# Kernel optimization log

Measured on AMD Instinct MI355X. Metric: run time of the kernel, lower is better.

## Reference

```python
import jax, jax.numpy as jnp
import numpy as np

B_SZ, SEQ, H, P = 4, 8192, 512, 256


def _s5(x, lam_re, lam_im, log_dt, b_re, b_im, c_re, c_im, d):
    """Single-direction S5 diagonal SSM. x: [B,L,H] -> y: [B,L,H]."""
    lam = lam_re + 1j * lam_im                      # [P] complex diagonal A
    dt = jnp.exp(log_dt)                            # [P] ZOH timestep
    a_bar = jnp.exp(lam * dt)                       # [P] discretized A
    b_bar = ((a_bar - 1.0) / lam)[:, None] * (b_re + 1j * b_im)  # [P,H]
    bu = jnp.einsum('blh,ph->blp', x.astype(b_bar.dtype), b_bar)  # [B,L,P]
    a_el = jnp.broadcast_to(a_bar, bu.shape)        # time-invariant A per step

    def comb(e1, e2):  # associative combine for linear recurrence
        a1, s1 = e1
        a2, s2 = e2
        return (a1 * a2, a2 * s1 + s2)

    _, states = jax.lax.associative_scan(comb, (a_el, bu), axis=1)  # [B,L,P]
    c = c_re + 1j * c_im                            # [H,P]
    return jnp.einsum('blp,hp->blh', states, c).real + x * d


def setup_inputs() -> dict:
    key = jax.random.key(0)
    ks = jax.random.split(key, 10)
    return {
        'x': jax.random.normal(ks[0], (B_SZ, SEQ, H), dtype=jnp.float32),
        'Lambda_re': -0.1 - 0.5 * jax.random.uniform(ks[1], (2, P), dtype=jnp.float32),
        'Lambda_im': jnp.pi * jax.random.normal(ks[2], (2, P), dtype=jnp.float32),
        'log_dt': jnp.log(0.001) + (jnp.log(0.1) - jnp.log(0.001)) * jax.random.uniform(ks[3], (2, P), dtype=jnp.float32),
        'B_re': jax.random.normal(ks[4], (2, P, H), dtype=jnp.float32) / np.sqrt(H),
        'B_im': jax.random.normal(ks[5], (2, P, H), dtype=jnp.float32) / np.sqrt(H),
        'C_re': jax.random.normal(ks[6], (2, H, P), dtype=jnp.float32) / np.sqrt(P),
        'C_im': jax.random.normal(ks[7], (2, H, P), dtype=jnp.float32) / np.sqrt(P),
        'D': jax.random.normal(ks[8], (2, H), dtype=jnp.float32),
    }


def reference(x, Lambda_re, Lambda_im, log_dt, B_re, B_im, C_re, C_im, D):
    # fwd(x) + flip(bwd(flip(x)))
    y_f = _s5(x, Lambda_re[0], Lambda_im[0], log_dt[0], B_re[0], B_im[0], C_re[0], C_im[0], D[0])
    x_r = x[:, ::-1]
    y_b = _s5(x_r, Lambda_re[1], Lambda_im[1], log_dt[1], B_re[1], B_im[1], C_re[1], C_im[1], D[1])[:, ::-1]
    return y_f + y_b
```

## Files before the change

kernel.cpp:

```cpp
#include <hip/hip_runtime.h>
#include <math.h>

typedef unsigned short ushort_t;
typedef __bf16 bf16x8 __attribute__((ext_vector_type(8)));
typedef ushort_t ushort8v __attribute__((ext_vector_type(8)));
typedef float f32x4 __attribute__((ext_vector_type(4)));

#define B_SZ   4
#define SEQ    8192
#define M_ROWS (B_SZ * SEQ)
#define CH     32
#define NC     (SEQ / CH)

__device__ __forceinline__ ushort_t f2bf(float f) {
    unsigned u = __float_as_uint(f);
    u = u + 0x7fffu + ((u >> 16) & 1u);
    return (ushort_t)(u >> 16);
}
__device__ __forceinline__ float bf2f(ushort_t b) {
    return __uint_as_float(((unsigned)b) << 16);
}

__device__ __forceinline__ void load16_lds(const void* g, void* l) {
    __builtin_amdgcn_global_load_lds(
        (const __attribute__((address_space(1))) unsigned int*)g,
        (__attribute__((address_space(3))) unsigned int*)l, 16, 0, 0);
}

__global__ void prep_kernel(const float* __restrict__ Lre,
                            const float* __restrict__ Lim,
                            const float* __restrict__ ldt,
                            const float* __restrict__ Bre,
                            const float* __restrict__ Bim,
                            const float* __restrict__ Cre,
                            const float* __restrict__ Cim,
                            float* __restrict__ abar,
                            float* __restrict__ apow,
                            ushort_t* __restrict__ Bmat,
                            ushort_t* __restrict__ Cmat) {
    int idx = blockIdx.x * 256 + threadIdx.x;
    int h = idx & 511;
    int p = (idx >> 9) & 255;
    int d = idx >> 17;
    int ip = d * 256 + p;
    float lr = Lre[ip], li = Lim[ip];
    float dt = expf(ldt[ip]);
    float e   = expf(lr * dt);
    float ang = li * dt;
    float ar = e * cosf(ang), ai = e * sinf(ang);
    float nr = ar - 1.0f, ni = ai;
    float den = lr * lr + li * li;
    float cr = (nr * lr + ni * li) / den;
    float ci = (ni * lr - nr * li) / den;
    float br = Bre[idx], bi = Bim[idx];
    Bmat[(d * 512 + 2 * p) * 512 + h]     = f2bf(cr * br - ci * bi);
    Bmat[(d * 512 + 2 * p + 1) * 512 + h] = f2bf(cr * bi + ci * br);
    if (h == 0) {
        int o = d * 512 + 2 * p;
        abar[o] = ar;  abar[o + 1] = ai;
        float eC = expf(lr * dt * (float)CH);
        float aC = ang * (float)CH;
        apow[o] = eC * cosf(aC);  apow[o + 1] = eC * sinf(aC);
    }
    int p2 = idx & 255;
    int h2 = (idx >> 8) & 511;
    int d2 = idx >> 17;
    Cmat[h2 * 1024 + d2 * 512 + 2 * p2]     = f2bf(Cre[idx]);
    Cmat[h2 * 1024 + d2 * 512 + 2 * p2 + 1] = f2bf(-Cim[idx]);
}

__global__ void conv_x_kernel(const float* __restrict__ x,
                              ushort_t* __restrict__ X16) {
    int i = blockIdx.x * 256 + threadIdx.x;
    float4 v = ((const float4*)x)[i];
    ushort_t o[4] = {f2bf(v.x), f2bf(v.y), f2bf(v.z), f2bf(v.w)};
    *(uint2*)&X16[(size_t)i * 4] = *(const uint2*)o;
}

template<int EPI, int KD_, int NT>
__global__ __launch_bounds__(256)
void gemm_mfma(const ushort_t* __restrict__ A, const ushort_t* __restrict__ Bm,
               ushort_t* __restrict__ Cb, float* __restrict__ Cf,
               const float* __restrict__ X, const float* __restrict__ Dv) {
    __shared__ ushort_t As[128 * 32];
    __shared__ ushort_t Bs[128 * 32];
    const int tid  = threadIdx.x;
    const int lane = tid & 63;
    const int wv   = tid >> 6;
    const int wrow = wv >> 1, wcol = wv & 1;
    const int l15  = lane & 15, lq = lane >> 4;

    const int lin = blockIdx.x;
    const int xcd = lin & 7;
    const int j   = lin >> 3;
    const int mt  = xcd * 32 + j / NT;
    const int nt  = j % NT;
    const int m0 = mt * 128;
    const int n0 = nt * 128;
    const int CN = NT * 128;

    f32x4 acc[4][4];
#pragma unroll
    for (int i = 0; i < 4; ++i)
#pragma unroll
        for (int jj = 0; jj < 4; ++jj)
            acc[i][jj] = (f32x4){0.f, 0.f, 0.f, 0.f};

    const int grow_l = lane >> 2;
    const int gk8    = (lane & 3) * 8;

    const ushort_t* aF = As + (wrow * 64 + l15) * 32 + lq * 8;
    const ushort_t* bF = Bs + (wcol * 64 + l15) * 32 + lq * 8;

    for (int kt = 0; kt < KD_; kt += 32) {
        __syncthreads();
#pragma unroll
        for (int j2 = 0; j2 < 2; ++j2) {
            const int r0 = j2 * 64 + wv * 16;
            load16_lds(&A[(size_t)(m0 + r0 + grow_l) * KD_ + kt + gk8],
                       (void*)&As[r0 * 32]);
            load16_lds(&Bm[(size_t)(n0 + r0 + grow_l) * KD_ + kt + gk8],
                       (void*)&Bs[r0 * 32]);
        }
        __syncthreads();

        bf16x8 af[4], bfr[4];
#pragma unroll
        for (int mi = 0; mi < 4; ++mi) {
            union { ushort8v u; bf16x8 b; } cv;
            cv.u = *(const ushort8v*)(aF + mi * 512);
            af[mi] = cv.b;
        }
#pragma unroll
        for (int ni = 0; ni < 4; ++ni) {
            union { ushort8v u; bf16x8 b; } cv;
            cv.u = *(const ushort8v*)(bF + ni * 512);
            bfr[ni] = cv.b;
        }
#pragma unroll
        for (int mi = 0; mi < 4; ++mi)
#pragma unroll
            for (int ni = 0; ni < 4; ++ni)
                acc[mi][ni] = __builtin_amdgcn_mfma_f32_16x16x32_bf16(
                    af[mi], bfr[ni], acc[mi][ni], 0, 0, 0);
    }

#pragma unroll
    for (int mi = 0; mi < 4; ++mi) {
#pragma unroll
        for (int ni = 0; ni < 4; ++ni) {
            const int col = n0 + wcol * 64 + ni * 16 + l15;
            float dsum = 0.f;
            if (EPI == 1) dsum = Dv[col] + Dv[512 + col];
#pragma unroll
            for (int r = 0; r < 4; ++r) {
                const int row = m0 + wrow * 64 + mi * 16 + lq * 4 + r;
                if (EPI == 0) {
                    Cb[(size_t)row * CN + col] = f2bf(acc[mi][ni][r]);
                } else {
                    const size_t idx = (size_t)row * 512 + col;
                    Cf[idx] = acc[mi][ni][r] + X[idx] * dsum;
                }
            }
        }
    }
}

__global__ __launch_bounds__(512)
void scan_carry(const ushort_t* __restrict__ S, const float* __restrict__ abar,
                float* __restrict__ carry) {
    int b = blockIdx.x, c = blockIdx.y, t = threadIdx.x;
    int dir = t >> 8, p = t & 255;
    float ar = abar[dir * 512 + 2 * p], ai = abar[dir * 512 + 2 * p + 1];
    float sr = 0.f, si = 0.f;
    const ushort_t* base = S + ((size_t)b * SEQ + (size_t)c * CH) * 1024
                             + dir * 512 + 2 * p;
    for (int batch = 0; batch < CH; batch += 8) {
        unsigned v[8];
#pragma unroll
        for (int q = 0; q < 8; ++q) {
            int l = batch + q;
            int row = dir ? (CH - 1 - l) : l;
            v[q] = *(const unsigned*)(base + (size_t)row * 1024);
        }
#pragma unroll
        for (int q = 0; q < 8; ++q) {
            float re = bf2f((ushort_t)(v[q] & 0xffffu));
            float im = bf2f((ushort_t)(v[q] >> 16));
            float nr = fmaf(ar, sr, fmaf(-ai, si, re));
            float ni = fmaf(ar, si, fmaf(ai, sr, im));
            sr = nr; si = ni;
        }
    }
    int o = (b * NC + c) * 1024 + dir * 512 + 2 * p;
    carry[o] = sr; carry[o + 1] = si;
}

__global__ __launch_bounds__(512)
void scan_comb(const float* __restrict__ carry, float* __restrict__ init,
               const float* __restrict__ apow) {
    int b = blockIdx.x, t = threadIdx.x;
    int dir = t >> 8, p = t & 255;
    float pr = apow[dir * 512 + 2 * p], pi = apow[dir * 512 + 2 * p + 1];
    float sr = 0.f, si = 0.f;
#pragma unroll 8
    for (int cc = 0; cc < NC; ++cc) {
        int c = dir ? (NC - 1 - cc) : cc;
        int o = (b * NC + c) * 1024 + dir * 512 + 2 * p;
        init[o] = sr; init[o + 1] = si;
        float cr = carry[o], ci = carry[o + 1];
        float nr = fmaf(pr, sr, fmaf(-pi, si, cr));
        float ni = fmaf(pr, si, fmaf(pi, sr, ci));
        sr = nr; si = ni;
    }
}

__global__ __launch_bounds__(512)
void scan_final(ushort_t* __restrict__ S, const float* __restrict__ abar,
                const float* __restrict__ init) {
    int b = blockIdx.x, c = blockIdx.y, t = threadIdx.x;
    int dir = t >> 8, p = t & 255;
    float ar = abar[dir * 512 + 2 * p], ai = abar[dir * 512 + 2 * p + 1];
    int o = (b * NC + c) * 1024 + dir * 512 + 2 * p;
    float sr = init[o], si = init[o + 1];
    ushort_t* base = S + ((size_t)b * SEQ + (size_t)c * CH) * 1024
                       + dir * 512 + 2 * p;
    for (int batch = 0; batch < CH; batch += 8) {
        unsigned v[8];
#pragma unroll
        for (int q = 0; q < 8; ++q) {
            int l = batch + q;
            int row = dir ? (CH - 1 - l) : l;
            v[q] = *(const unsigned*)(base + (size_t)row * 1024);
        }
#pragma unroll
        for (int q = 0; q < 8; ++q) {
            float re = bf2f((ushort_t)(v[q] & 0xffffu));
            float im = bf2f((ushort_t)(v[q] >> 16));
            float nr = fmaf(ar, sr, fmaf(-ai, si, re));
            float ni = fmaf(ar, si, fmaf(ai, sr, im));
            sr = nr; si = ni;
            v[q] = ((unsigned)f2bf(si) << 16) | (unsigned)f2bf(sr);
        }
#pragma unroll
        for (int q = 0; q < 8; ++q) {
            int l = batch + q;
            int row = dir ? (CH - 1 - l) : l;
            *(unsigned*)(base + (size_t)row * 1024) = v[q];
        }
    }
}

extern "C" void kernel_launch(void* const* d_in, const int* in_sizes, int n_in,
                              void* d_out, int out_size, void* d_ws, size_t ws_size,
                              hipStream_t stream) {
    const float* x   = (const float*)d_in[0];
    const float* Lre = (const float*)d_in[1];
    const float* Lim = (const float*)d_in[2];
    const float* ldt = (const float*)d_in[3];
    const float* Bre = (const float*)d_in[4];
    const float* Bim = (const float*)d_in[5];
    const float* Cre = (const float*)d_in[6];
    const float* Cim = (const float*)d_in[7];
    const float* Dv  = (const float*)d_in[8];
    float* y = (float*)d_out;
    char* ws = (char*)d_ws;

    ushort_t* SB   = (ushort_t*)(ws);
    ushort_t* Bm16 = (ushort_t*)(ws + 67108864);
    ushort_t* Cm16 = (ushort_t*)(ws + 68157440);
    float* abar  = (float*)(ws + 69206016);
    float* apow  = (float*)(ws + 69210112);
    ushort_t* X16  = (ushort_t*)(ws + 69214208);
    float* carry = (float*)(ws + 69214208);
    float* initb = (float*)(ws + 73408512);

    prep_kernel<<<1024, 256, 0, stream>>>(Lre, Lim, ldt, Bre, Bim, Cre, Cim,
                                          abar, apow, Bm16, Cm16);
    conv_x_kernel<<<16384, 256, 0, stream>>>(x, X16);

    gemm_mfma<0, 512, 8><<<2048, 256, 0, stream>>>(X16, Bm16, SB, nullptr,
                                                   nullptr, nullptr);

    dim3 gs(B_SZ, NC);
    scan_carry<<<gs, 512, 0, stream>>>(SB, abar, carry);
    scan_comb<<<B_SZ, 512, 0, stream>>>(carry, initb, apow);
    scan_final<<<gs, 512, 0, stream>>>(SB, abar, initb);

    gemm_mfma<1, 1024, 4><<<1024, 256, 0, stream>>>(SB, Cm16, nullptr, y,
                                                    x, Dv);
}
```

Measured before the change: 298.7 us.

## Fuse chunk-carry scan into first GEMM epilogue and merge prep kernels

Fuses the per-chunk carry scan into the first GEMM's epilogue. Results are staged in LDS, each 32-row chunk is scanned from LDS, and SB is written with coalesced 16-byte stores. This removes the separate scan_carry pass that re-read SB from global memory. The prep and x-conversion kernels are merged into one launch, and the second GEMM stages its output through LDS for vectorized float4 stores with the D skip term. The carry buffer now lives in the output buffer, and the added LDS staging raises per-block shared memory use.

```diff
diff --git a/kernel.cpp b/kernel.cpp
--- a/kernel.cpp
+++ b/kernel.cpp
@@ -8,9 +8,11 @@
 
 #define B_SZ   4
 #define SEQ    8192
-#define M_ROWS (B_SZ * SEQ)
+#define M_ROWS 32768
 #define CH     32
-#define NC     (SEQ / CH)
+#define NC     256
+#define SSTR   136
+#define FSTR   132
 
 __device__ __forceinline__ ushort_t f2bf(float f) {
     unsigned u = __float_as_uint(f);
@@ -27,63 +29,61 @@
         (__attribute__((address_space(3))) unsigned int*)l, 16, 0, 0);
 }
 
-__global__ void prep_kernel(const float* __restrict__ Lre,
-                            const float* __restrict__ Lim,
-                            const float* __restrict__ ldt,
-                            const float* __restrict__ Bre,
-                            const float* __restrict__ Bim,
-                            const float* __restrict__ Cre,
-                            const float* __restrict__ Cim,
-                            float* __restrict__ abar,
-                            float* __restrict__ apow,
-                            ushort_t* __restrict__ Bmat,
-                            ushort_t* __restrict__ Cmat) {
-    int idx = blockIdx.x * 256 + threadIdx.x;
-    int h = idx & 511;
-    int p = (idx >> 9) & 255;
-    int d = idx >> 17;
-    int ip = d * 256 + p;
-    float lr = Lre[ip], li = Lim[ip];
-    float dt = expf(ldt[ip]);
-    float e   = expf(lr * dt);
-    float ang = li * dt;
-    float ar = e * cosf(ang), ai = e * sinf(ang);
-    float nr = ar - 1.0f, ni = ai;
-    float den = lr * lr + li * li;
-    float cr = (nr * lr + ni * li) / den;
-    float ci = (ni * lr - nr * li) / den;
-    float br = Bre[idx], bi = Bim[idx];
-    Bmat[(d * 512 + 2 * p) * 512 + h]     = f2bf(cr * br - ci * bi);
-    Bmat[(d * 512 + 2 * p + 1) * 512 + h] = f2bf(cr * bi + ci * br);
-    if (h == 0) {
-        int o = d * 512 + 2 * p;
-        abar[o] = ar;  abar[o + 1] = ai;
-        float eC = expf(lr * dt * (float)CH);
-        float aC = ang * (float)CH;
-        apow[o] = eC * cosf(aC);  apow[o + 1] = eC * sinf(aC);
-    }
-    int p2 = idx & 255;
-    int h2 = (idx >> 8) & 511;
-    int d2 = idx >> 17;
-    Cmat[h2 * 1024 + d2 * 512 + 2 * p2]     = f2bf(Cre[idx]);
-    Cmat[h2 * 1024 + d2 * 512 + 2 * p2 + 1] = f2bf(-Cim[idx]);
-}
-
-__global__ void conv_x_kernel(const float* __restrict__ x,
-                              ushort_t* __restrict__ X16) {
+__global__ __launch_bounds__(256)
+void prep_conv(const float* __restrict__ x, ushort_t* __restrict__ X16,
+               const float* __restrict__ Lre, const float* __restrict__ Lim,
+               const float* __restrict__ ldt,
+               const float* __restrict__ Bre, const float* __restrict__ Bim,
+               const float* __restrict__ Cre, const float* __restrict__ Cim,
+               float* __restrict__ abar, float* __restrict__ apow,
+               ushort_t* __restrict__ Bmat, ushort_t* __restrict__ Cmat) {
     int i = blockIdx.x * 256 + threadIdx.x;
     float4 v = ((const float4*)x)[i];
     ushort_t o[4] = {f2bf(v.x), f2bf(v.y), f2bf(v.z), f2bf(v.w)};
     *(uint2*)&X16[(size_t)i * 4] = *(const uint2*)o;
-}
-
-template<int EPI, int KD_, int NT>
+
+    if (blockIdx.x < 1024) {
+        int idx = i;
+        int h = idx & 511;
+        int p = (idx >> 9) & 255;
+        int d = idx >> 17;
+        int ip = d * 256 + p;
+        float lr = Lre[ip], li = Lim[ip];
+        float dt = expf(ldt[ip]);
+        float e   = expf(lr * dt);
+        float ang = li * dt;
+        float ar = e * cosf(ang), ai = e * sinf(ang);
+        float nr = ar - 1.0f, ni = ai;
+        float den = lr * lr + li * li;
+        float cr = (nr * lr + ni * li) / den;
+        float ci = (ni * lr - nr * li) / den;
+        float br = Bre[idx], bi = Bim[idx];
+        Bmat[(d * 512 + 2 * p) * 512 + h]     = f2bf(cr * br - ci * bi);
+        Bmat[(d * 512 + 2 * p + 1) * 512 + h] = f2bf(cr * bi + ci * br);
+        if (h == 0) {
+            int oo = d * 512 + 2 * p;
+            abar[oo] = ar;  abar[oo + 1] = ai;
+            float eC = expf(lr * dt * (float)CH);
+            float aC = ang * (float)CH;
+            apow[oo] = eC * cosf(aC);  apow[oo + 1] = eC * sinf(aC);
+        }
+        int p2 = idx & 255;
+        int h2 = (idx >> 8) & 511;
+        int d2 = idx >> 17;
+        Cmat[h2 * 1024 + d2 * 512 + 2 * p2]     = f2bf(Cre[idx]);
+        Cmat[h2 * 1024 + d2 * 512 + 2 * p2 + 1] = f2bf(-Cim[idx]);
+    }
+}
+
 __global__ __launch_bounds__(256)
-void gemm_mfma(const ushort_t* __restrict__ A, const ushort_t* __restrict__ Bm,
-               ushort_t* __restrict__ Cb, float* __restrict__ Cf,
-               const float* __restrict__ X, const float* __restrict__ Dv) {
-    __shared__ ushort_t As[128 * 32];
-    __shared__ ushort_t Bs[128 * 32];
+void gemm1_mfma(const ushort_t* __restrict__ A, const ushort_t* __restrict__ Bm,
+                ushort_t* __restrict__ SB, const float* __restrict__ abar,
+                float* __restrict__ carry) {
+    __shared__ __align__(16) char lds[128 * SSTR * 2];
+    ushort_t* As = (ushort_t*)lds;
+    ushort_t* Bs = (ushort_t*)(lds + 8192);
+    ushort_t* scanbuf = (ushort_t*)lds;
+
     const int tid  = threadIdx.x;
     const int lane = tid & 63;
     const int wv   = tid >> 6;
@@ -93,11 +93,10 @@
     const int lin = blockIdx.x;
     const int xcd = lin & 7;
     const int j   = lin >> 3;
-    const int mt  = xcd * 32 + j / NT;
-    const int nt  = j % NT;
+    const int mt  = xcd * 32 + (j >> 3);
+    const int nt  = j & 7;
     const int m0 = mt * 128;
     const int n0 = nt * 128;
-    const int CN = NT * 128;
 
     f32x4 acc[4][4];
 #pragma unroll
@@ -108,18 +107,17 @@
 
     const int grow_l = lane >> 2;
     const int gk8    = (lane & 3) * 8;
-
     const ushort_t* aF = As + (wrow * 64 + l15) * 32 + lq * 8;
     const ushort_t* bF = Bs + (wcol * 64 + l15) * 32 + lq * 8;
 
-    for (int kt = 0; kt < KD_; kt += 32) {
+    for (int kt = 0; kt < 512; kt += 32) {
         __syncthreads();
 #pragma unroll
         for (int j2 = 0; j2 < 2; ++j2) {
             const int r0 = j2 * 64 + wv * 16;
-            load16_lds(&A[(size_t)(m0 + r0 + grow_l) * KD_ + kt + gk8],
+            load16_lds(&A[(size_t)(m0 + r0 + grow_l) * 512 + kt + gk8],
                        (void*)&As[r0 * 32]);
-            load16_lds(&Bm[(size_t)(n0 + r0 + grow_l) * KD_ + kt + gk8],
+            load16_lds(&Bm[(size_t)(n0 + r0 + grow_l) * 512 + kt + gk8],
                        (void*)&Bs[r0 * 32]);
         }
         __syncthreads();
@@ -145,55 +143,52 @@
                     af[mi], bfr[ni], acc[mi][ni], 0, 0, 0);
     }
 
-#pragma unroll
-    for (int mi = 0; mi < 4; ++mi) {
+    __syncthreads();
+#pragma unroll
+    for (int mi = 0; mi < 4; ++mi)
 #pragma unroll
         for (int ni = 0; ni < 4; ++ni) {
-            const int col = n0 + wcol * 64 + ni * 16 + l15;
-            float dsum = 0.f;
-            if (EPI == 1) dsum = Dv[col] + Dv[512 + col];
+            const int col = wcol * 64 + ni * 16 + l15;
 #pragma unroll
             for (int r = 0; r < 4; ++r) {
-                const int row = m0 + wrow * 64 + mi * 16 + lq * 4 + r;
-                if (EPI == 0) {
-                    Cb[(size_t)row * CN + col] = f2bf(acc[mi][ni][r]);
-                } else {
-                    const size_t idx = (size_t)row * 512 + col;
-                    Cf[idx] = acc[mi][ni][r] + X[idx] * dsum;
-                }
+                const int row = wrow * 64 + mi * 16 + lq * 4 + r;
+                scanbuf[row * SSTR + col] = f2bf(acc[mi][ni][r]);
             }
         }
-    }
-}
-
-__global__ __launch_bounds__(512)
-void scan_carry(const ushort_t* __restrict__ S, const float* __restrict__ abar,
-                float* __restrict__ carry) {
-    int b = blockIdx.x, c = blockIdx.y, t = threadIdx.x;
-    int dir = t >> 8, p = t & 255;
-    float ar = abar[dir * 512 + 2 * p], ai = abar[dir * 512 + 2 * p + 1];
-    float sr = 0.f, si = 0.f;
-    const ushort_t* base = S + ((size_t)b * SEQ + (size_t)c * CH) * 1024
-                             + dir * 512 + 2 * p;
-    for (int batch = 0; batch < CH; batch += 8) {
-        unsigned v[8];
-#pragma unroll
-        for (int q = 0; q < 8; ++q) {
-            int l = batch + q;
-            int row = dir ? (CH - 1 - l) : l;
-            v[q] = *(const unsigned*)(base + (size_t)row * 1024);
-        }
-#pragma unroll
-        for (int q = 0; q < 8; ++q) {
-            float re = bf2f((ushort_t)(v[q] & 0xffffu));
-            float im = bf2f((ushort_t)(v[q] >> 16));
+    __syncthreads();
+
+    {
+        const int row = tid >> 1, hf = tid & 1;
+        const ushort_t* src = scanbuf + row * SSTR + hf * 64;
+        ushort_t* dst = SB + (size_t)(m0 + row) * 1024 + n0 + hf * 64;
+        const int rot = ((row >> 3) << 1) & 7;
+#pragma unroll
+        for (int q0 = 0; q0 < 8; ++q0) {
+            int q = (q0 + rot) & 7;
+            *(ushort8v*)(dst + q * 8) = *(const ushort8v*)(src + q * 8);
+        }
+    }
+
+    {
+        const int ch = tid & 63, sg = tid >> 6;
+        const int pg = (n0 >> 1) + ch;
+        const bool bwd = (n0 >= 512);
+        const float ar = abar[2 * pg], ai = abar[2 * pg + 1];
+        float sr = 0.f, si = 0.f;
+#pragma unroll 8
+        for (int i2 = 0; i2 < 32; ++i2) {
+            const int row = sg * 32 + (bwd ? 31 - i2 : i2);
+            unsigned u = *(const unsigned*)&scanbuf[row * SSTR + 2 * ch];
+            float re = bf2f((ushort_t)(u & 0xffffu));
+            float im = bf2f((ushort_t)(u >> 16));
             float nr = fmaf(ar, sr, fmaf(-ai, si, re));
             float ni = fmaf(ar, si, fmaf(ai, sr, im));
             sr = nr; si = ni;
         }
-    }
-    int o = (b * NC + c) * 1024 + dir * 512 + 2 * p;
-    carry[o] = sr; carry[o + 1] = si;
+        const int ms = (m0 >> 5) + sg;
+        carry[ms * 1024 + 2 * pg]     = sr;
+        carry[ms * 1024 + 2 * pg + 1] = si;
+    }
 }
 
 __global__ __launch_bounds__(512)
@@ -251,6 +246,112 @@
     }
 }
 
+__global__ __launch_bounds__(256)
+void gemm2_mfma(const ushort_t* __restrict__ A, const ushort_t* __restrict__ Bm,
+                float* __restrict__ y, const float* __restrict__ X,
+                const float* __restrict__ Dv) {
+    __shared__ __align__(16) char lds[34816];
+    ushort_t* As = (ushort_t*)lds;
+    ushort_t* Bs = (ushort_t*)(lds + 8192);
+    float* fscan = (float*)lds;
+    float* dsum  = (float*)(lds + 33792);
+
+    const int tid  = threadIdx.x;
+    const int lane = tid & 63;
+    const int wv   = tid >> 6;
+    const int wrow = wv >> 1, wcol = wv & 1;
+    const int l15  = lane & 15, lq = lane >> 4;
+
+    const int lin = blockIdx.x;
+    const int xcd = lin & 7;
+    const int j   = lin >> 3;
+    const int mt  = xcd * 32 + (j >> 2);
+    const int nt  = j & 3;
+    const int m0 = mt * 128;
+    const int n0 = nt * 128;
+
+    if (tid < 128) dsum[tid] = Dv[n0 + tid] + Dv[512 + n0 + tid];
+
+    f32x4 acc[4][4];
+#pragma unroll
+    for (int i = 0; i < 4; ++i)
+#pragma unroll
+        for (int jj = 0; jj < 4; ++jj)
+            acc[i][jj] = (f32x4){0.f, 0.f, 0.f, 0.f};
+
+    const int grow_l = lane >> 2;
+    const int gk8    = (lane & 3) * 8;
+    const ushort_t* aF = As + (wrow * 64 + l15) * 32 + lq * 8;
+    const ushort_t* bF = Bs + (wcol * 64 + l15) * 32 + lq * 8;
+
+    for (int kt = 0; kt < 1024; kt += 32) {
+        __syncthreads();
+#pragma unroll
+        for (int j2 = 0; j2 < 2; ++j2) {
+            const int r0 = j2 * 64 + wv * 16;
+            load16_lds(&A[(size_t)(m0 + r0 + grow_l) * 1024 + kt + gk8],
+                       (void*)&As[r0 * 32]);
+            load16_lds(&Bm[(size_t)(n0 + r0 + grow_l) * 1024 + kt + gk8],
+                       (void*)&Bs[r0 * 32]);
+        }
+        __syncthreads();
+
+        bf16x8 af[4], bfr[4];
+#pragma unroll
+        for (int mi = 0; mi < 4; ++mi) {
+            union { ushort8v u; bf16x8 b; } cv;
+            cv.u = *(const ushort8v*)(aF + mi * 512);
+            af[mi] = cv.b;
+        }
+#pragma unroll
+        for (int ni = 0; ni < 4; ++ni) {
+            union { ushort8v u; bf16x8 b; } cv;
+            cv.u = *(const ushort8v*)(bF + ni * 512);
+            bfr[ni] = cv.b;
+        }
+#pragma unroll
+        for (int mi = 0; mi < 4; ++mi)
+#pragma unroll
+            for (int ni = 0; ni < 4; ++ni)
+                acc[mi][ni] = __builtin_amdgcn_mfma_f32_16x16x32_bf16(
+                    af[mi], bfr[ni], acc[mi][ni], 0, 0, 0);
+    }
+
+#pragma unroll
+    for (int h = 0; h < 2; ++h) {
+        __syncthreads();
+        if (wrow == h) {
+#pragma unroll
+            for (int mi = 0; mi < 4; ++mi)
+#pragma unroll
+                for (int ni = 0; ni < 4; ++ni) {
+                    const int col = wcol * 64 + ni * 16 + l15;
+#pragma unroll
+                    for (int r = 0; r < 4; ++r)
+                        fscan[(mi * 16 + lq * 4 + r) * FSTR + col] =
+                            acc[mi][ni][r];
+                }
+        }
+        __syncthreads();
+        const int rl = tid >> 2, q = tid & 3;
+        const float* src = fscan + rl * FSTR + q * 32;
+        const size_t gbase = (size_t)(m0 + h * 64 + rl) * 512 + n0 + q * 32;
+#pragma unroll
+        for (int c0 = 0; c0 < 8; ++c0) {
+            int c = (c0 + 2 * q) & 7;
+            f32x4 v  = *(const f32x4*)(src + c * 4);
+            float4 xv = *(const float4*)&X[gbase + c * 4];
+            f32x4 dv = *(const f32x4*)(dsum + q * 32 + c * 4);
+            float4 o;
+            o.x = v[0] + xv.x * dv[0];
+            o.y = v[1] + xv.y * dv[1];
+            o.z = v[2] + xv.z * dv[2];
+            o.w = v[3] + xv.w * dv[3];
+            *(float4*)&y[gbase + c * 4] = o;
+        }
+    }
+}
+
 extern "C" void kernel_launch(void* const* d_in, const int* in_sizes, int n_in,
                               void* d_out, int out_size, void* d_ws, size_t ws_size,
                               hipStream_t stream) {
@@ -272,21 +373,18 @@
     float* abar  = (float*)(ws + 69206016);
     float* apow  = (float*)(ws + 69210112);
     ushort_t* X16  = (ushort_t*)(ws + 69214208);
-    float* carry = (float*)(ws + 69214208);
-    float* initb = (float*)(ws + 73408512);
-
-    prep_kernel<<<1024, 256, 0, stream>>>(Lre, Lim, ldt, Bre, Bim, Cre, Cim,
-                                          abar, apow, Bm16, Cm16);
-    conv_x_kernel<<<16384, 256, 0, stream>>>(x, X16);
-
-    gemm_mfma<0, 512, 8><<<2048, 256, 0, stream>>>(X16, Bm16, SB, nullptr,
-                                                   nullptr, nullptr);
+    float* initb = (float*)(ws + 69214208);
+    float* carry = (float*)d_out;
+
+    prep_conv<<<16384, 256, 0, stream>>>(x, X16, Lre, Lim, ldt, Bre, Bim,
+                                         Cre, Cim, abar, apow, Bm16, Cm16);
+
+    gemm1_mfma<<<2048, 256, 0, stream>>>(X16, Bm16, SB, abar, carry);
+
+    scan_comb<<<B_SZ, 512, 0, stream>>>(carry, initb, apow);
 
     dim3 gs(B_SZ, NC);
-    scan_carry<<<gs, 512, 0, stream>>>(SB, abar, carry);
-    scan_comb<<<B_SZ, 512, 0, stream>>>(carry, initb, apow);
     scan_final<<<gs, 512, 0, stream>>>(SB, abar, initb);
 
-    gemm_mfma<1, 1024, 4><<<1024, 256, 0, stream>>>(SB, Cm16, nullptr, y,
-                                                    x, Dv);
-}
+    gemm2_mfma<<<1024, 256, 0, stream>>>(SB, Cm16, y, x, Dv);
+}
```

New measurement: 311.4 us. +4.2%, slower.
